# Optimization experiments

Hardware: AMD Instinct MI355X
Metric: run time of the kernel (lower is better)

Reference implementation:

```python
import jax, jax.numpy as jnp
import numpy as np
from jax import lax

HIDDEN = 50


def setup_inputs() -> dict:
    key = jax.random.key(0)
    ks = jax.random.split(key, 8)
    B, T, I, H, O = 8192, 256, 1, HIDDEN, 1
    s = 0.1  # small init scale, keeps tanh/sigmoid in a sane range
    return {
        "x": jax.random.normal(ks[0], (B, T, I), dtype=jnp.float32),
        "W_ih": jax.random.normal(ks[1], (4 * H, I), dtype=jnp.float32) * s,
        "W_hh": jax.random.normal(ks[2], (4 * H, H), dtype=jnp.float32) * s,
        "b_ih": jax.random.normal(ks[3], (4 * H,), dtype=jnp.float32) * s,
        "b_hh": jax.random.normal(ks[4], (4 * H,), dtype=jnp.float32) * s,
        "W_lin": jax.random.normal(ks[5], (O, H), dtype=jnp.float32) * s,
        "b_lin": jax.random.normal(ks[6], (O,), dtype=jnp.float32) * s,
    }


def reference(x, W_ih, W_hh, b_ih, b_hh, W_lin, b_lin):
    # Single-layer batch_first LSTM; PyTorch gate order is (i, f, g, o).
    # lstm_out[:, -1] == final hidden state h_T for num_layers=1, so we only
    # carry (h, c) and never materialize the full [B, T, H] output.
    # Dropout is identity in eval mode.
    B = x.shape[0]
    b = b_ih + b_hh  # [4H]

    def step(carry, x_t):
        h, c = carry  # [B, H] each
        gates = x_t @ W_ih.T + h @ W_hh.T + b  # [B, 4H]
        i, f, g, o = jnp.split(gates, 4, axis=-1)
        i = jax.nn.sigmoid(i)
        f = jax.nn.sigmoid(f)
        g = jnp.tanh(g)
        o = jax.nn.sigmoid(o)
        c = f * c + i * g
        h = o * jnp.tanh(c)
        return (h, c), None

    xs = jnp.swapaxes(x, 0, 1)  # [T, B, I]
    h0 = jnp.zeros((B, HIDDEN), dtype=x.dtype)
    (hT, _), _ = lax.scan(step, (h0, h0), xs)
    return hT @ W_lin.T + b_lin  # [B, output_size]
```

## Files before the change

kernel.cpp:

```cpp
#include <hip/hip_runtime.h>


#define NTH 896
#define TST 256
#define MB 16
#define NBLK 512
#define HR 72
#define HSZ (MB * HR)

#define LOG2E 1.44269504088896f

typedef __attribute__((ext_vector_type(8))) _Float16 half8;
typedef __attribute__((ext_vector_type(4))) float float4v;

__device__ __forceinline__ float rcp_(float v)  { return __builtin_amdgcn_rcpf(v); }
__device__ __forceinline__ float exp2_(float v) { return __builtin_amdgcn_exp2f(v); }
__device__ __forceinline__ unsigned short f16bits(float v) {
    _Float16 h = (_Float16)v;
    return *(unsigned short*)&h;
}

__global__ __launch_bounds__(NTH, 7) void lstm_mfma(
    const float* __restrict__ x,
    const float* __restrict__ W_ih,
    const float* __restrict__ W_hh,
    const float* __restrict__ b_ih,
    const float* __restrict__ b_hh,
    const float* __restrict__ W_lin,
    const float* __restrict__ b_lin,
    float* __restrict__ out)
{
    __shared__ __align__(16) unsigned short Hh[2 * HSZ];

    const int tid  = threadIdx.x;
    const int wv   = tid >> 6;
    const int ln   = tid & 63;
    const int lrow = ln & 15;
    const int quad = ln >> 4;
    const int bbase = (int)blockIdx.x * MB;
    const int T = wv;

    half8 wh[2];
    {
        const int gr = T * 16 + lrow;
        const int j  = gr >> 2, g = gr & 3;
        const int row = g * 50 + j;
        const float scl = (g == 2) ? (2.0f * LOG2E) : (-LOG2E);
        #pragma unroll
        for (int q2 = 0; q2 < 2; ++q2) {
            half8 h8;
            #pragma unroll
            for (int i = 0; i < 8; ++i) {
                const int k = q2 * 32 + quad * 8 + i;
                float V = 0.0f;
                if (j < 50) {
                    if (k < 50)       V = W_hh[row * 50 + k];
                    else if (k == 50) V = W_ih[row];
                    else if (k == 51) V = b_ih[row] + b_hh[row];
                }
                h8[i] = (_Float16)(V * scl);
            }
            wh[q2] = h8;
        }
    }

    for (int i = tid; i < HSZ; i += NTH)
        ((unsigned int*)Hh)[i] = 0u;
    __syncthreads();
    if (tid < MB) {
        float xv = x[(bbase + tid) * TST + 0];
        Hh[tid * HR + 50] = f16bits(xv);
        Hh[tid * HR + 51] = 0x3C00;
        Hh[HSZ + tid * HR + 51] = 0x3C00;
    }
    __syncthreads();

    float c2 = 0.0f;
    const unsigned short* Hr = &Hh[lrow * HR + quad * 8];
    int jw = T * 4 + quad;
    if (jw >= 50) jw = 52 + quad;
    unsigned short* Hw = &Hh[lrow * HR + jw];
    const float* xr = &x[(bbase + lrow) * TST];
    const float4v z4 = {0.f, 0.f, 0.f, 0.f};

    auto step1 = [&](int roff, int woff) {
        const half8 b0 = *(const half8*)(Hr + roff);
        const half8 b1 = *(const half8*)(Hr + roff + 32);

        float4v a4;
        a4 = __builtin_amdgcn_mfma_f32_16x16x32_f16(wh[0], b0, z4, 0, 0, 0);
        a4 = __builtin_amdgcn_mfma_f32_16x16x32_f16(wh[1], b1, a4, 0, 0, 0);

        const float Ei = exp2_(a4[0]);
        const float Ef = exp2_(a4[1]);
        const float Eg = exp2_(a4[2]);
        const float Eo = exp2_(a4[3]);
        const float D1 = 1.0f + Ef;
        const float D2 = (Eg + 1.0f) * (1.0f + Ei);
        const float R  = rcp_(D1 * D2);
        const float tg = (Eg - 1.0f) * D1;
        const float nm = fmaf(2.0f * LOG2E, tg, c2 * D2);
        c2 = fminf(nm * R, 120.0f);
        const float Ec = exp2_(c2);
        const float R2 = rcp_((Ec + 1.0f) * (1.0f + Eo));
        const float hn = (Ec - 1.0f) * R2;

        Hw[woff] = f16bits(hn);
    };

    #pragma unroll 1
    for (int t2 = 0; t2 < TST / 2; ++t2) {
        if (wv == 13) {
            const float xA = xr[2 * t2 + 1];
            const float xB = xr[(2 * t2 + 2) & 255];
            if (ln < 16)
                Hh[HSZ + lrow * HR + 50] = f16bits(xA);
            __syncthreads();
            if (ln < 16)
                Hh[lrow * HR + 50] = f16bits(xB);
            __syncthreads();
        } else {
            step1(0, HSZ);
            __syncthreads();
            step1(HSZ, 0);
            __syncthreads();
        }
    }

    if (tid < MB) {
        float s = b_lin[0];
        #pragma unroll 10
        for (int k = 0; k < 50; ++k) {
            float hk = (float)(*(const _Float16*)&Hh[tid * HR + k]);
            s += hk * W_lin[k];
        }
        out[bbase + tid] = s;
    }
}

extern "C" void kernel_launch(void* const* d_in, const int* in_sizes, int n_in,
                              void* d_out, int out_size, void* d_ws, size_t ws_size,
                              hipStream_t stream) {
    const float* x     = (const float*)d_in[0];
    const float* W_ih  = (const float*)d_in[1];
    const float* W_hh  = (const float*)d_in[2];
    const float* b_ih  = (const float*)d_in[3];
    const float* b_hh  = (const float*)d_in[4];
    const float* W_lin = (const float*)d_in[5];
    const float* b_lin = (const float*)d_in[6];
    float* out = (float*)d_out;

    lstm_mfma<<<dim3(NBLK), dim3(NTH), 0, stream>>>(
        x, W_ih, W_hh, b_ih, b_hh, W_lin, b_lin, out);
}
```

Before: 208.4 us.

## Halve block size: each wave computes two gate tiles, fold x-loader into compute wave

Measured after the change: 216.0 us. 3.7% more time.

```diff
diff --git a/kernel.cpp b/kernel.cpp
--- a/kernel.cpp
+++ b/kernel.cpp
@@ -1,7 +1,7 @@
 #include <hip/hip_runtime.h>
 
 
-#define NTH 896
+#define NTH 448
 #define TST 256
 #define MB 16
 #define NBLK 512
@@ -20,7 +20,7 @@
     return *(unsigned short*)&h;
 }
 
-__global__ __launch_bounds__(NTH, 7) void lstm_mfma(
+__global__ __launch_bounds__(NTH, 4) void lstm_mfma(
     const float* __restrict__ x,
     const float* __restrict__ W_ih,
     const float* __restrict__ W_hh,
@@ -38,30 +38,37 @@
     const int lrow = ln & 15;
     const int quad = ln >> 4;
     const int bbase = (int)blockIdx.x * MB;
-    const int T = wv;
+    const bool w6 = (wv == 6);
+    const int TA = w6 ? 12 : 2 * wv;
+    const int TB = 2 * wv + 1;
 
-    half8 wh[2];
+    half8 whA[2], whB[2];
     {
-        const int gr = T * 16 + lrow;
-        const int j  = gr >> 2, g = gr & 3;
-        const int row = g * 50 + j;
-        const float scl = (g == 2) ? (2.0f * LOG2E) : (-LOG2E);
-        #pragma unroll
-        for (int q2 = 0; q2 < 2; ++q2) {
-            half8 h8;
+        auto fill = [&](int T, half8* dst) {
+            const int gr = T * 16 + lrow;
+            const int j  = gr >> 2, g = gr & 3;
+            const int row = g * 50 + j;
+            const float scl = (g == 2) ? (2.0f * LOG2E) : (-LOG2E);
             #pragma unroll
-            for (int i = 0; i < 8; ++i) {
-                const int k = q2 * 32 + quad * 8 + i;
-                float V = 0.0f;
-                if (j < 50) {
-                    if (k < 50)       V = W_hh[row * 50 + k];
-                    else if (k == 50) V = W_ih[row];
-                    else if (k == 51) V = b_ih[row] + b_hh[row];
+            for (int q2 = 0; q2 < 2; ++q2) {
+                half8 h8;
+                #pragma unroll
+                for (int i = 0; i < 8; ++i) {
+                    const int k = q2 * 32 + quad * 8 + i;
+                    float V = 0.0f;
+                    if (j < 50) {
+                        if (k < 50)       V = W_hh[row * 50 + k];
+                        else if (k == 50) V = W_ih[row];
+                        else if (k == 51) V = b_ih[row] + b_hh[row];
+                    }
+                    h8[i] = (_Float16)(V * scl);
                 }
-                h8[i] = (_Float16)(V * scl);
+                dst[q2] = h8;
             }
-            wh[q2] = h8;
-        }
+        };
+        fill(TA, whA);
+        if (!w6) fill(TB, whB);
+        else     { whB[0] = whA[0]; whB[1] = whA[1]; }
     }
 
     for (int i = tid; i < HSZ; i += NTH)
@@ -75,22 +82,17 @@
     }
     __syncthreads();
 
-    float c2 = 0.0f;
+    float c2A = 0.0f, c2B = 0.0f;
     const unsigned short* Hr = &Hh[lrow * HR + quad * 8];
-    int jw = T * 4 + quad;
-    if (jw >= 50) jw = 52 + quad;
-    unsigned short* Hw = &Hh[lrow * HR + jw];
+    int jwA = TA * 4 + quad;
+    if (jwA >= 50) jwA = 52 + quad;
+    const int jwB = TB * 4 + quad;
+    unsigned short* HwA = &Hh[lrow * HR + jwA];
+    unsigned short* HwB = &Hh[lrow * HR + jwB];
     const float* xr = &x[(bbase + lrow) * TST];
     const float4v z4 = {0.f, 0.f, 0.f, 0.f};
 
-    auto step1 = [&](int roff, int woff) {
-        const half8 b0 = *(const half8*)(Hr + roff);
-        const half8 b1 = *(const half8*)(Hr + roff + 32);
-
-        float4v a4;
-        a4 = __builtin_amdgcn_mfma_f32_16x16x32_f16(wh[0], b0, z4, 0, 0, 0);
-        a4 = __builtin_amdgcn_mfma_f32_16x16x32_f16(wh[1], b1, a4, 0, 0, 0);
-
+    auto act = [&](const float4v a4, float& c2) -> unsigned short {
         const float Ei = exp2_(a4[0]);
         const float Ef = exp2_(a4[1]);
         const float Eg = exp2_(a4[2]);
@@ -103,28 +105,39 @@
         c2 = fminf(nm * R, 120.0f);
         const float Ec = exp2_(c2);
         const float R2 = rcp_((Ec + 1.0f) * (1.0f + Eo));
-        const float hn = (Ec - 1.0f) * R2;
+        return f16bits((Ec - 1.0f) * R2);
+    };
 
-        Hw[woff] = f16bits(hn);
+    auto step2 = [&](int roff, int woff) {
+        const half8 b0 = *(const half8*)(Hr + roff);
+        const half8 b1 = *(const half8*)(Hr + roff + 32);
+
+        float4v aA = __builtin_amdgcn_mfma_f32_16x16x32_f16(whA[0], b0, z4, 0, 0, 0);
+        aA = __builtin_amdgcn_mfma_f32_16x16x32_f16(whA[1], b1, aA, 0, 0, 0);
+        float4v aB = __builtin_amdgcn_mfma_f32_16x16x32_f16(whB[0], b0, z4, 0, 0, 0);
+        aB = __builtin_amdgcn_mfma_f32_16x16x32_f16(whB[1], b1, aB, 0, 0, 0);
+
+        HwA[woff] = act(aA, c2A);
+        if (!w6) HwB[woff] = act(aB, c2B);
     };
 
     #pragma unroll 1
     for (int t2 = 0; t2 < TST / 2; ++t2) {
-        if (wv == 13) {
-            const float xA = xr[2 * t2 + 1];
-            const float xB = xr[(2 * t2 + 2) & 255];
-            if (ln < 16)
-                Hh[HSZ + lrow * HR + 50] = f16bits(xA);
-            __syncthreads();
-            if (ln < 16)
-                Hh[lrow * HR + 50] = f16bits(xB);
-            __syncthreads();
-        } else {
-            step1(0, HSZ);
-            __syncthreads();
-            step1(HSZ, 0);
-            __syncthreads();
+        float xA = 0.0f, xB = 0.0f;
+        if (w6 && ln < 16) {
+            xA = xr[2 * t2 + 1];
+            xB = xr[(2 * t2 + 2) & 255];
         }
+
+        step2(0, HSZ);
+        if (w6 && ln < 16)
+            Hh[HSZ + lrow * HR + 50] = f16bits(xA);
+        __syncthreads();
+
+        step2(HSZ, 0);
+        if (w6 && ln < 16)
+            Hh[lrow * HR + 50] = f16bits(xB);
+        __syncthreads();
     }
 
     if (tid < MB) {
```

## Interleave two batch groups per block to overlap MFMA with activation math

Applied to the files above, without the earlier changes.

After: 232.8 us. 1.12x slower.

```diff
diff --git a/kernel.cpp b/kernel.cpp
--- a/kernel.cpp
+++ b/kernel.cpp
@@ -3,10 +3,15 @@
 
 #define NTH 896
 #define TST 256
-#define MB 16
-#define NBLK 512
+#define MBG 16
+#define NBLK 256
 #define HR 72
-#define HSZ (MB * HR)
+#define HSZ (MBG * HR)
+
+#define A0O 0
+#define A1O HSZ
+#define B0O (2 * HSZ)
+#define B1O (3 * HSZ)
 
 #define LOG2E 1.44269504088896f
 
@@ -20,7 +25,7 @@
     return *(unsigned short*)&h;
 }
 
-__global__ __launch_bounds__(NTH, 7) void lstm_mfma(
+__global__ __launch_bounds__(NTH, 4) void lstm_mfma(
     const float* __restrict__ x,
     const float* __restrict__ W_ih,
     const float* __restrict__ W_hh,
@@ -30,14 +35,14 @@
     const float* __restrict__ b_lin,
     float* __restrict__ out)
 {
-    __shared__ __align__(16) unsigned short Hh[2 * HSZ];
+    __shared__ __align__(16) unsigned short Hh[4 * HSZ];
 
     const int tid  = threadIdx.x;
     const int wv   = tid >> 6;
     const int ln   = tid & 63;
     const int lrow = ln & 15;
     const int quad = ln >> 4;
-    const int bbase = (int)blockIdx.x * MB;
+    const int bbase = (int)blockIdx.x * (2 * MBG);
     const int T = wv;
 
     half8 wh[2];
@@ -64,33 +69,31 @@
         }
     }
 
-    for (int i = tid; i < HSZ; i += NTH)
+    for (int i = tid; i < 2 * HSZ; i += NTH)
         ((unsigned int*)Hh)[i] = 0u;
     __syncthreads();
-    if (tid < MB) {
-        float xv = x[(bbase + tid) * TST + 0];
-        Hh[tid * HR + 50] = f16bits(xv);
-        Hh[tid * HR + 51] = 0x3C00;
-        Hh[HSZ + tid * HR + 51] = 0x3C00;
+    if (tid < 2 * MBG) {
+        const int g = tid >> 4, r = tid & 15;
+        const float xv = x[(bbase + tid) * TST + 0];
+        Hh[(g ? B0O : A0O) + r * HR + 50] = f16bits(xv);
+    }
+    if (tid < MBG) {
+        #pragma unroll
+        for (int p = 0; p < 4; ++p)
+            Hh[p * HSZ + tid * HR + 51] = 0x3C00;
     }
     __syncthreads();
 
-    float c2 = 0.0f;
-    const unsigned short* Hr = &Hh[lrow * HR + quad * 8];
+    float c2A = 0.0f, c2B = 0.0f;
+    const unsigned short* HrP = &Hh[lrow * HR + quad * 8];
     int jw = T * 4 + quad;
     if (jw >= 50) jw = 52 + quad;
     unsigned short* Hw = &Hh[lrow * HR + jw];
-    const float* xr = &x[(bbase + lrow) * TST];
+    const float* xrA = &x[(bbase + lrow) * TST];
+    const float* xrB = &x[(bbase + MBG + lrow) * TST];
     const float4v z4 = {0.f, 0.f, 0.f, 0.f};
 
-    auto step1 = [&](int roff, int woff) {
-        const half8 b0 = *(const half8*)(Hr + roff);
-        const half8 b1 = *(const half8*)(Hr + roff + 32);
-
-        float4v a4;
-        a4 = __builtin_amdgcn_mfma_f32_16x16x32_f16(wh[0], b0, z4, 0, 0, 0);
-        a4 = __builtin_amdgcn_mfma_f32_16x16x32_f16(wh[1], b1, a4, 0, 0, 0);
-
+    auto act = [&](const float4v a4, float& c2) -> unsigned short {
         const float Ei = exp2_(a4[0]);
         const float Ef = exp2_(a4[1]);
         const float Eg = exp2_(a4[2]);
@@ -103,35 +106,61 @@
         c2 = fminf(nm * R, 120.0f);
         const float Ec = exp2_(c2);
         const float R2 = rcp_((Ec + 1.0f) * (1.0f + Eo));
-        const float hn = (Ec - 1.0f) * R2;
+        return f16bits((Ec - 1.0f) * R2);
+    };
 
-        Hw[woff] = f16bits(hn);
+    auto hstep = [&](int roff, int woff, float4v& gIn, float& c2, float4v& gOut) {
+        const half8 b0 = *(const half8*)(HrP + roff);
+        const half8 b1 = *(const half8*)(HrP + roff + 32);
+        const unsigned short hb = act(gIn, c2);
+        float4v a4 = __builtin_amdgcn_mfma_f32_16x16x32_f16(wh[0], b0, z4, 0, 0, 0);
+        a4 = __builtin_amdgcn_mfma_f32_16x16x32_f16(wh[1], b1, a4, 0, 0, 0);
+        gOut = a4;
+        Hw[woff] = hb;
     };
+
+    float4v gA = z4, gB = z4;
+    if (wv != 13) {
+        const half8 b0 = *(const half8*)(HrP + A0O);
+        const half8 b1 = *(const half8*)(HrP + A0O + 32);
+        gA = __builtin_amdgcn_mfma_f32_16x16x32_f16(wh[0], b0, z4, 0, 0, 0);
+        gA = __builtin_amdgcn_mfma_f32_16x16x32_f16(wh[1], b1, gA, 0, 0, 0);
+    }
 
     #pragma unroll 1
     for (int t2 = 0; t2 < TST / 2; ++t2) {
         if (wv == 13) {
-            const float xA = xr[2 * t2 + 1];
-            const float xB = xr[(2 * t2 + 2) & 255];
-            if (ln < 16)
-                Hh[HSZ + lrow * HR + 50] = f16bits(xA);
+            const float xa1 = xrA[2 * t2 + 1];
+            const float xb1 = xrB[2 * t2 + 1];
+            const float xa2 = xrA[(2 * t2 + 2) & 255];
+            const float xb2 = xrB[(2 * t2 + 2) & 255];
+            if (ln < 16) Hh[A1O + lrow * HR + 50] = f16bits(xa1);
             __syncthreads();
-            if (ln < 16)
-                Hh[lrow * HR + 50] = f16bits(xB);
+            if (ln < 16) Hh[B1O + lrow * HR + 50] = f16bits(xb1);
+            __syncthreads();
+            if (ln < 16) Hh[A0O + lrow * HR + 50] = f16bits(xa2);
+            __syncthreads();
+            if (ln < 16) Hh[B0O + lrow * HR + 50] = f16bits(xb2);
             __syncthreads();
         } else {
-            step1(0, HSZ);
+            hstep(B0O, A1O, gA, c2A, gB);
             __syncthreads();
-            step1(HSZ, 0);
+            hstep(A1O, B1O, gB, c2B, gA);
+            __syncthreads();
+            hstep(B1O, A0O, gA, c2A, gB);
+            __syncthreads();
+            hstep(A0O, B0O, gB, c2B, gA);
             __syncthreads();
         }
     }
 
-    if (tid < MB) {
+    if (tid < 2 * MBG) {
+        const int g = tid >> 4, r = tid & 15;
+        const unsigned short* hp = &Hh[(g ? B0O : A0O) + r * HR];
         float s = b_lin[0];
         #pragma unroll 10
         for (int k = 0; k < 50; ++k) {
-            float hk = (float)(*(const _Float16*)&Hh[tid * HR + k]);
+            float hk = (float)(*(const _Float16*)&hp[k]);
             s += hk * W_lin[k];
         }
         out[bbase + tid] = s;
```

## Replace gate exp2 with packed polynomial and prefetch x one step ahead

Applied to the files above, without the earlier changes.

New measurement: 272.4 us. 30.7% more time.

```diff
diff --git a/kernel.cpp b/kernel.cpp
--- a/kernel.cpp
+++ b/kernel.cpp
@@ -12,12 +12,35 @@
 
 typedef __attribute__((ext_vector_type(8))) _Float16 half8;
 typedef __attribute__((ext_vector_type(4))) float float4v;
+typedef __attribute__((ext_vector_type(2))) float f2;
 
 __device__ __forceinline__ float rcp_(float v)  { return __builtin_amdgcn_rcpf(v); }
 __device__ __forceinline__ float exp2_(float v) { return __builtin_amdgcn_exp2f(v); }
 __device__ __forceinline__ unsigned short f16bits(float v) {
     _Float16 h = (_Float16)v;
     return *(unsigned short*)&h;
+}
+
+__device__ __forceinline__ f2 exp2p(f2 x) {
+    f2 kf;
+    kf.x = __builtin_rintf(x.x);
+    kf.y = __builtin_rintf(x.y);
+    const f2 f = x - kf;
+    const float C1 = 0.69314718056f, C2 = 0.24022650700f,
+                C3 = 0.05550410866f, C4 = 0.00961812911f,
+                C5 = 0.00133335581f;
+    f2 p = (f2){C5, C5};
+    p = __builtin_elementwise_fma(p, f, (f2){C4, C4});
+    p = __builtin_elementwise_fma(p, f, (f2){C3, C3});
+    p = __builtin_elementwise_fma(p, f, (f2){C2, C2});
+    p = __builtin_elementwise_fma(p, f, (f2){C1, C1});
+    p = __builtin_elementwise_fma(p, f, (f2){1.0f, 1.0f});
+    const int e0 = ((int)kf.x + 127) << 23;
+    const int e1 = ((int)kf.y + 127) << 23;
+    f2 s;
+    s.x = __builtin_bit_cast(float, e0);
+    s.y = __builtin_bit_cast(float, e1);
+    return p * s;
 }
 
 __global__ __launch_bounds__(NTH, 7) void lstm_mfma(
@@ -83,6 +106,9 @@
     const float* xr = &x[(bbase + lrow) * TST];
     const float4v z4 = {0.f, 0.f, 0.f, 0.f};
 
+    float pA = 0.0f, pB = 0.0f;
+    if (wv == 13) { pA = xr[1]; pB = xr[2]; }
+
     auto step1 = [&](int roff, int woff) {
         const half8 b0 = *(const half8*)(Hr + roff);
         const half8 b1 = *(const half8*)(Hr + roff + 32);
@@ -91,18 +117,19 @@
         a4 = __builtin_amdgcn_mfma_f32_16x16x32_f16(wh[0], b0, z4, 0, 0, 0);
         a4 = __builtin_amdgcn_mfma_f32_16x16x32_f16(wh[1], b1, a4, 0, 0, 0);
 
-        const float Ei = exp2_(a4[0]);
-        const float Ef = exp2_(a4[1]);
-        const float Eg = exp2_(a4[2]);
-        const float Eo = exp2_(a4[3]);
-        const float D1 = 1.0f + Ef;
-        const float D2 = (Eg + 1.0f) * (1.0f + Ei);
-        const float R  = rcp_(D1 * D2);
-        const float tg = (Eg - 1.0f) * D1;
+        f2 g01; g01.x = a4[0]; g01.y = a4[1];
+        f2 g23; g23.x = a4[2]; g23.y = a4[3];
+        const f2 P1 = exp2p(g01);
+        const f2 P2 = exp2p(g23);
+        const f2 Q1 = P1 + 1.0f;
+        const f2 Q2 = P2 + 1.0f;
+        const float D2 = Q2.x * Q1.x;
+        const float R  = rcp_(Q1.y * D2);
+        const float tg = (P2.x - 1.0f) * Q1.y;
         const float nm = fmaf(2.0f * LOG2E, tg, c2 * D2);
         c2 = fminf(nm * R, 120.0f);
         const float Ec = exp2_(c2);
-        const float R2 = rcp_((Ec + 1.0f) * (1.0f + Eo));
+        const float R2 = rcp_((Ec + 1.0f) * Q2.y);
         const float hn = (Ec - 1.0f) * R2;
 
         Hw[woff] = f16bits(hn);
@@ -111,14 +138,15 @@
     #pragma unroll 1
     for (int t2 = 0; t2 < TST / 2; ++t2) {
         if (wv == 13) {
-            const float xA = xr[2 * t2 + 1];
-            const float xB = xr[(2 * t2 + 2) & 255];
+            const float nA = xr[(2 * t2 + 3) & 255];
+            const float nB = xr[(2 * t2 + 4) & 255];
             if (ln < 16)
-                Hh[HSZ + lrow * HR + 50] = f16bits(xA);
+                Hh[HSZ + lrow * HR + 50] = f16bits(pA);
             __syncthreads();
             if (ln < 16)
-                Hh[lrow * HR + 50] = f16bits(xB);
+                Hh[lrow * HR + 50] = f16bits(pB);
             __syncthreads();
+            pA = nA; pB = nB;
         } else {
             step1(0, HSZ);
             __syncthreads();
```
